# Kernel tuning notes

Hardware: AMD Instinct MI355X
Metric: run time of the kernel (lower is better)

Reference implementation:

```python
import jax, jax.numpy as jnp
import numpy as np

B, F, N, L, K = 16, 256, 16384, 4096, 9  # batch, channels, input pixels, pooled pixels, kernel


def setup_inputs() -> dict:
    key = jax.random.key(0)
    k1, k2 = jax.random.split(key, 2)
    input_images = jax.random.normal(k1, (B, F, N), dtype=jnp.float32)
    # raw indices in [-1, N-1]; -1 marks a missing neighbor (zero padding)
    raw = jax.random.randint(k2, (L, K), 0, N + 1) - 1
    mask = (raw != -1).astype(jnp.float32)          # prepare_mask: mask out -1 entries
    indices = jnp.maximum(raw, 0)                   # prepare_mask: clamp -1 -> 0
    return {"input_images": input_images, "indices": indices, "mask": mask}


def reference(input_images, indices, mask):
    # gather neighbor features: (B, F, L, K)
    col = input_images[..., indices] * mask
    # max over kernel (neighbor) axis -> pooled image (B, F, L)
    return jnp.max(col, axis=-1)
```

## Files before the change

kernel.cpp:

```cpp
#include <hip/hip_runtime.h>

#define B_ 16
#define F_ 256
#define N_ 16384
#define L_ 4096
#define K_ 9

#define NTHR 256
#define NPAIR (B_ * F_ / 2)

__global__ __launch_bounds__(256) void prep_comb_kernel(
    const int* __restrict__ idx, const float* __restrict__ mask,
    unsigned short* __restrict__ comb) {
  int t = blockIdx.x * blockDim.x + threadIdx.x;
  if (t >= L_ * K_) return;
  int l = t / K_;
  int k = t - l * K_;
  comb[k * L_ + l] =
      (mask[t] != 0.0f) ? (unsigned short)idx[t] : (unsigned short)N_;
}

__device__ __forceinline__ unsigned bf16rn(float x) {
  unsigned u = __float_as_uint(x);
  return (u + 0x7fffu + ((u >> 16) & 1u)) >> 16;
}
__device__ __forceinline__ unsigned pack2(float a, float b) {
  return bf16rn(a) | (bf16rn(b) << 16);
}

__global__ __launch_bounds__(NTHR) void pool_pair_kernel(
    const float* __restrict__ img, const unsigned short* __restrict__ comb,
    float* __restrict__ out) {
  __shared__ __align__(16) unsigned pairbuf[N_ + 4];
  const int pid = blockIdx.x;
  const int tid = threadIdx.x;

  const float4* A4 = (const float4*)(img + (size_t)(2 * pid) * N_);
  const float4* B4 = (const float4*)(img + (size_t)(2 * pid + 1) * N_);
  uint4* dst4 = (uint4*)pairbuf;
#pragma unroll
  for (int i = 0; i < (N_ / 4) / NTHR; ++i) {
    int j = i * NTHR + tid;
    float4 a = A4[j];
    float4 b = B4[j];
    uint4 w;
    w.x = pack2(a.x, b.x);
    w.y = pack2(a.y, b.y);
    w.z = pack2(a.z, b.z);
    w.w = pack2(a.w, b.w);
    dst4[j] = w;
  }
  if (tid == 0) pairbuf[N_] = 0u;
  __syncthreads();

  float* outA = out + (size_t)(2 * pid) * L_;
  float* outB = outA + L_;
#pragma unroll 4
  for (int it = 0; it < L_ / NTHR; ++it) {
    int l = it * NTHR + tid;
    float ma = -INFINITY, mb = -INFINITY;
#pragma unroll
    for (int k = 0; k < K_; ++k) {
      unsigned id = comb[k * L_ + l];
      unsigned w = pairbuf[id];
      ma = fmaxf(ma, __uint_as_float(w << 16));
      mb = fmaxf(mb, __uint_as_float(w & 0xffff0000u));
    }
    outA[l] = ma;
    outB[l] = mb;
  }
}

__global__ __launch_bounds__(256) void pool_kernel_direct(
    const float* __restrict__ img, const int* __restrict__ idx,
    const float* __restrict__ mask, float* __restrict__ out) {
  __shared__ __align__(16) float row[N_ + 4];
  const int bf = blockIdx.x;
  const int tid = threadIdx.x;

  const float4* src4 = (const float4*)(img + (size_t)bf * N_);
  float4* row4 = (float4*)row;
#pragma unroll
  for (int i = 0; i < 16; ++i) {
    int j = i * 256 + tid;
    row4[j] = src4[j];
  }
  __syncthreads();

  float* outp = out + (size_t)bf * L_;
  for (int it = 0; it < L_ / 256; ++it) {
    int l = it * 256 + tid;
    float m = -INFINITY;
#pragma unroll
    for (int k = 0; k < K_; ++k) {
      int t = l * K_ + k;
      float v = (mask[t] != 0.0f) ? row[idx[t]] : 0.0f;
      m = fmaxf(m, v);
    }
    outp[l] = m;
  }
}

extern "C" void kernel_launch(void* const* d_in, const int* in_sizes, int n_in,
                              void* d_out, int out_size, void* d_ws, size_t ws_size,
                              hipStream_t stream) {
  const float* img = (const float*)d_in[0];
  const int* idx = (const int*)d_in[1];
  const float* mask = (const float*)d_in[2];
  float* out = (float*)d_out;

  const size_t comb_bytes = (size_t)L_ * K_ * sizeof(unsigned short);
  if (ws_size >= comb_bytes) {
    unsigned short* comb = (unsigned short*)d_ws;
    int total = L_ * K_;
    prep_comb_kernel<<<(total + 255) / 256, 256, 0, stream>>>(idx, mask, comb);
    pool_pair_kernel<<<NPAIR, NTHR, 0, stream>>>(img, comb, out);
  } else {
    pool_kernel_direct<<<B_ * F_, 256, 0, stream>>>(img, idx, mask, out);
  }
}
```

Before: 80.89 us.

## Use persistent producer/consumer blocks with double-buffered shared rows

Replaces one-block-per-channel-pair with 256 persistent 1024-thread blocks. Within each block, half the threads load and pack the next channel pair into a second shared buffer while the other half gather and max-pool the current pair. The aim is to overlap global loads with the shared-memory gather phase. In exchange it uses about 128KB of LDS per block, so only one block fits per CU, and it adds a block-wide barrier after every pair.

Measured after the change: 173.2 us. 114% more time.

```diff
diff --git a/kernel.cpp b/kernel.cpp
--- a/kernel.cpp
+++ b/kernel.cpp
@@ -6,8 +6,10 @@
 #define L_ 4096
 #define K_ 9
 
-#define NTHR 256
+#define NTHR 1024
+#define NBLK 256
 #define NPAIR (B_ * F_ / 2)
+#define PPB (NPAIR / NBLK)
 
 __global__ __launch_bounds__(256) void prep_comb_kernel(
     const int* __restrict__ idx, const float* __restrict__ mask,
@@ -28,46 +30,78 @@
   return bf16rn(a) | (bf16rn(b) << 16);
 }
 
-__global__ __launch_bounds__(NTHR) void pool_pair_kernel(
+__global__ __launch_bounds__(NTHR) void pool_pc_kernel(
     const float* __restrict__ img, const unsigned short* __restrict__ comb,
     float* __restrict__ out) {
-  __shared__ __align__(16) unsigned pairbuf[N_ + 4];
-  const int pid = blockIdx.x;
+  __shared__ __align__(16) unsigned buf[2][N_ + 4];
   const int tid = threadIdx.x;
+  const int bid = blockIdx.x;
+  const bool producer = tid < 512;
 
-  const float4* A4 = (const float4*)(img + (size_t)(2 * pid) * N_);
-  const float4* B4 = (const float4*)(img + (size_t)(2 * pid + 1) * N_);
-  uint4* dst4 = (uint4*)pairbuf;
+  if (tid < 2) buf[tid][N_] = 0u;
+
+  if (producer) {
+    const int pid = bid * PPB;
+    const float4* A4 = (const float4*)(img + (size_t)(2 * pid) * N_);
+    const float4* B4 = A4 + (N_ / 4);
 #pragma unroll
-  for (int i = 0; i < (N_ / 4) / NTHR; ++i) {
-    int j = i * NTHR + tid;
-    float4 a = A4[j];
-    float4 b = B4[j];
-    uint4 w;
-    w.x = pack2(a.x, b.x);
-    w.y = pack2(a.y, b.y);
-    w.z = pack2(a.z, b.z);
-    w.w = pack2(a.w, b.w);
-    dst4[j] = w;
+    for (int i = 0; i < 8; ++i) {
+      int j = tid + i * 512;
+      float4 a = A4[j];
+      float4 b = B4[j];
+      uint4 w;
+      w.x = pack2(a.x, b.x);
+      w.y = pack2(a.y, b.y);
+      w.z = pack2(a.z, b.z);
+      w.w = pack2(a.w, b.w);
+      *(uint4*)(&buf[0][4 * j]) = w;
+    }
   }
-  if (tid == 0) pairbuf[N_] = 0u;
   __syncthreads();
 
-  float* outA = out + (size_t)(2 * pid) * L_;
-  float* outB = outA + L_;
-#pragma unroll 4
-  for (int it = 0; it < L_ / NTHR; ++it) {
-    int l = it * NTHR + tid;
-    float ma = -INFINITY, mb = -INFINITY;
+#pragma unroll 1
+  for (int p = 0; p < PPB; ++p) {
+    if (producer) {
+      if (p + 1 < PPB) {
+        const int pid = bid * PPB + p + 1;
+        const int s = (p + 1) & 1;
+        const float4* A4 = (const float4*)(img + (size_t)(2 * pid) * N_);
+        const float4* B4 = A4 + (N_ / 4);
 #pragma unroll
-    for (int k = 0; k < K_; ++k) {
-      unsigned id = comb[k * L_ + l];
-      unsigned w = pairbuf[id];
-      ma = fmaxf(ma, __uint_as_float(w << 16));
-      mb = fmaxf(mb, __uint_as_float(w & 0xffff0000u));
+        for (int i = 0; i < 8; ++i) {
+          int j = tid + i * 512;
+          float4 a = A4[j];
+          float4 b = B4[j];
+          uint4 w;
+          w.x = pack2(a.x, b.x);
+          w.y = pack2(a.y, b.y);
+          w.z = pack2(a.z, b.z);
+          w.w = pack2(a.w, b.w);
+          *(uint4*)(&buf[s][4 * j]) = w;
+        }
+      }
+    } else {
+      const int pid = bid * PPB + p;
+      const int s = p & 1;
+      const int cl = tid - 512;
+      float* outA = out + (size_t)(2 * pid) * L_;
+      float* outB = outA + L_;
+#pragma unroll
+      for (int it = 0; it < L_ / 512; ++it) {
+        int l = cl + it * 512;
+        float ma = -INFINITY, mb = -INFINITY;
+#pragma unroll
+        for (int k = 0; k < K_; ++k) {
+          unsigned id = comb[k * L_ + l];
+          unsigned w = buf[s][id];
+          ma = fmaxf(ma, __uint_as_float(w << 16));
+          mb = fmaxf(mb, __uint_as_float(w & 0xffff0000u));
+        }
+        outA[l] = ma;
+        outB[l] = mb;
+      }
     }
-    outA[l] = ma;
-    outB[l] = mb;
+    __syncthreads();
   }
 }
 
@@ -114,7 +148,7 @@
     unsigned short* comb = (unsigned short*)d_ws;
     int total = L_ * K_;
     prep_comb_kernel<<<(total + 255) / 256, 256, 0, stream>>>(idx, mask, comb);
-    pool_pair_kernel<<<NPAIR, NTHR, 0, stream>>>(img, comb, out);
+    pool_pc_kernel<<<NBLK, NTHR, 0, stream>>>(img, comb, out);
   } else {
     pool_kernel_direct<<<B_ * F_, 256, 0, stream>>>(img, idx, mask, out);
   }
```
